# Kernel tuning notes

Measured on AMD Instinct MI355X. Metric: run time of the kernel, lower is better.

The kernel has to match this reference:

```python
import jax, jax.numpy as jnp
import numpy as np

N_MBED = 384
HEAD_SIZE = 64

def setup_inputs() -> dict:
    key = jax.random.key(0)
    kx, kq, kk, kv = jax.random.split(key, 4)
    B, T = 128, 256
    x = jax.random.normal(kx, (B, T, N_MBED), dtype=jnp.float32)
    # torch nn.Linear(n_mbed, head_size, bias=False): y = x @ W^T, W:[head_size, n_mbed].
    # We store the transposed weight [n_mbed, head_size] so y = x @ W.
    s = 1.0 / np.sqrt(N_MBED)
    Wq = jax.random.uniform(kq, (N_MBED, HEAD_SIZE), jnp.float32, -s, s)
    Wk = jax.random.uniform(kk, (N_MBED, HEAD_SIZE), jnp.float32, -s, s)
    Wv = jax.random.uniform(kv, (N_MBED, HEAD_SIZE), jnp.float32, -s, s)
    return {"x": x, "Wq": Wq, "Wk": Wk, "Wv": Wv}

def reference(x, Wq, Wk, Wv):
    B, T, C = x.shape  # C = n_mbed = 384
    q = x @ Wq  # [B,T,H]
    k = x @ Wk
    v = x @ Wv
    # Faithful to source: wei = k @ q^T, scaled by C**-0.5 (C = n_mbed, not head_size)
    wei = jnp.einsum('bth,bsh->bts', k, q) * (C ** -0.5)  # [B,T,T]
    mask = jnp.tril(jnp.ones((T, T), dtype=bool))
    wei = jnp.where(mask, wei, -jnp.inf)
    wei = jax.nn.softmax(wei, axis=-1)
    # dropout omitted (eval mode / identity)
    out = jnp.einsum('bts,bsh->bth', wei, v)  # [B,T,H]
    return out
```

## Files before the change

### kernel.cpp

```cpp
#include <hip/hip_runtime.h>
#include <hip/hip_bf16.h>
#include <math.h>

constexpr int kB = 128;
constexpr int kT = 256;
constexpr int kC = 384;
constexpr int kH = 64;

using bf16x8 = __attribute__((ext_vector_type(8))) short;
using f32x4  = __attribute__((ext_vector_type(4))) float;

union BF8 { bf16x8 v; __hip_bfloat162 h[4]; };
union BF4 { short4 s; __hip_bfloat162 h[2]; };

__device__ inline bf16x8 cvt8(float4 a, float4 b) {
    BF8 u;
    u.h[0] = __float22bfloat162_rn(float2{a.x, a.y});
    u.h[1] = __float22bfloat162_rn(float2{a.z, a.w});
    u.h[2] = __float22bfloat162_rn(float2{b.x, b.y});
    u.h[3] = __float22bfloat162_rn(float2{b.z, b.w});
    return u.v;
}
__device__ inline short4 cvt4(float4 a) {
    BF4 u;
    u.h[0] = __float22bfloat162_rn(float2{a.x, a.y});
    u.h[1] = __float22bfloat162_rn(float2{a.z, a.w});
    return u.s;
}
__device__ inline short bf1(float f) {
    __hip_bfloat16 h = __float2bfloat16(f);
    return *(short*)&h;
}

__global__ void prep_kernel(const float* __restrict__ Wq,
                            const float* __restrict__ Wk,
                            const float* __restrict__ Wv,
                            __hip_bfloat16* __restrict__ Wt) {
    int idx = blockIdx.x * 256 + threadIdx.x;
    int n = idx / kC, c = idx % kC;
    int w = n >> 6, h = n & 63;
    const float* W = (w == 0) ? Wq : (w == 1) ? Wk : Wv;
    float val = W[c * kH + h];
    if (w == 1) val *= 0.051031036307982884f;
    Wt[idx] = __float2bfloat16(val);
}

__global__ __launch_bounds__(512, 2) void fused_kernel(
    const float* __restrict__ x, const __hip_bfloat16* __restrict__ Wt,
    float* __restrict__ out)
{
    __shared__ short Qs[256 * 72];
    __shared__ short Ks[128 * 72];
    __shared__ short VTs[64 * 264];
    __shared__ short As[2][256 * 36];
    __shared__ short Bs[2][192 * 36];

    const int b    = blockIdx.y;
    const int half = (int)blockIdx.x ^ 1;
    const int t0   = half * 128;

    const int tid  = threadIdx.x;
    const int wave = tid >> 6, lane = tid & 63;
    const int m16  = lane & 15, quad = lane >> 4;
    const int wm = wave & 1, wn = wave >> 1;
    const short* wt = (const short*)Wt;
    const float* xb = x + (size_t)b * kT * kC;

    const bool mfmaAct = (half == 1) || (wm == 0);

    const int arow = tid >> 1, acol = (tid & 1) * 16;
    const bool aAct = (half == 1) || (arow < 128);

    float4 la[4]; bf16x8 lb0, lb1;
    auto glod = [&](int k0) {
        if (aAct) {
#pragma unroll
            for (int i = 0; i < 4; ++i)
                la[i] = *(const float4*)(xb + (size_t)arow * kC + k0 + acol + 4 * i);
        }
        {
            int n = tid >> 2, kk = (tid & 3) * 8;
            lb0 = *(const bf16x8*)(wt + (size_t)n * kC + k0 + kk);
        }
        if (tid < 256) {
            int c = tid + 512;
            int n = c >> 2, kk = (c & 3) * 8;
            lb1 = *(const bf16x8*)(wt + (size_t)n * kC + k0 + kk);
        }
    };
    auto swr = [&](int d) {
        if (aAct) {
#pragma unroll
            for (int i = 0; i < 4; ++i)
                *(short4*)&As[d][arow * 36 + acol + 4 * i] = cvt4(la[i]);
        }
        {
            int n = tid >> 2, kk = (tid & 3) * 8;
            *(bf16x8*)&Bs[d][n * 36 + kk] = lb0;
        }
        if (tid < 256) {
            int c = tid + 512;
            int n = c >> 2, kk = (c & 3) * 8;
            *(bf16x8*)&Bs[d][n * 36 + kk] = lb1;
        }
    };

    f32x4 acc[8][3];
#pragma unroll
    for (int mt = 0; mt < 8; ++mt)
#pragma unroll
        for (int j = 0; j < 3; ++j) acc[mt][j] = f32x4{0.f, 0.f, 0.f, 0.f};

    glod(0);
    swr(0);
    __syncthreads();

    for (int s = 0; s < 12; ++s) {
        const int d = s & 1;
        if (s < 11) glod((s + 1) * 32);

        if (mfmaAct) {
            bf16x8 af[8], bfr[3];
#pragma unroll
            for (int j = 0; j < 3; ++j)
                bfr[j] = *(const bf16x8*)&Bs[d][((wn * 3 + j) * 16 + m16) * 36 + quad * 8];
#pragma unroll
            for (int mt = 0; mt < 8; ++mt)
                af[mt] = *(const bf16x8*)&As[d][(wm * 128 + mt * 16 + m16) * 36 + quad * 8];
#pragma unroll
            for (int mt = 0; mt < 8; ++mt)
#pragma unroll
                for (int j = 0; j < 3; ++j)
                    acc[mt][j] = __builtin_amdgcn_mfma_f32_16x16x32_bf16(
                        af[mt], bfr[j], acc[mt][j], 0, 0, 0);
        }

        if (s < 11) swr(d ^ 1);
        __syncthreads();
    }

    if (mfmaAct) {
#pragma unroll
        for (int mt = 0; mt < 8; ++mt) {
            const int mbase = wm * 128 + mt * 16 + quad * 4;
#pragma unroll
            for (int j = 0; j < 3; ++j) {
                const int nt = wn * 3 + j;
                const int w  = nt >> 2;
                const int h  = (nt & 3) * 16 + m16;
                if (w == 2) {
                    float4 f = make_float4(acc[mt][j][0], acc[mt][j][1],
                                           acc[mt][j][2], acc[mt][j][3]);
                    *(short4*)&VTs[h * 264 + mbase] = cvt4(f);
                } else if (w == 1) {
                    if ((mbase >> 7) == half) {
#pragma unroll
                        for (int r = 0; r < 4; ++r)
                            Ks[(mbase + r - t0) * 72 + h] = bf1(acc[mt][j][r]);
                    }
                } else {
#pragma unroll
                    for (int r = 0; r < 4; ++r)
                        Qs[(mbase + r) * 72 + h] = bf1(acc[mt][j][r]);
                }
            }
        }
    }
    __syncthreads();

    const int wband = t0 + wave * 16;
    float* Pw = (float*)(&As[0][0]) + wave * 16 * 68;

    const bf16x8 ka0 = *(const bf16x8*)&Ks[(wave * 16 + m16) * 72 + quad * 8];
    const bf16x8 ka1 = *(const bf16x8*)&Ks[(wave * 16 + m16) * 72 + quad * 8 + 32];

    f32x4 O[4];
    float m_[4], l_[4];
#pragma unroll
    for (int i = 0; i < 4; ++i) {
        O[i] = f32x4{0.f, 0.f, 0.f, 0.f};
        m_[i] = -INFINITY; l_[i] = 0.f;
    }

    const int ilast = wband >> 6;
    for (int i = 0; i <= ilast; ++i) {
        const bool diag = (i == ilast);
        const int jmax = diag ? (wave & 3) : 3;

        f32x4 S[4];
        const f32x4 Z = f32x4{0.f, 0.f, 0.f, 0.f};
#pragma unroll
        for (int j = 0; j < 4; ++j) {
            if (j <= jmax) {
                bf16x8 qb0 = *(const bf16x8*)&Qs[(i * 64 + j * 16 + m16) * 72 + quad * 8];
                bf16x8 qb1 = *(const bf16x8*)&Qs[(i * 64 + j * 16 + m16) * 72 + quad * 8 + 32];
                S[j] = __builtin_amdgcn_mfma_f32_16x16x32_bf16(ka0, qb0, Z, 0, 0, 0);
                S[j] = __builtin_amdgcn_mfma_f32_16x16x32_bf16(ka1, qb1, S[j], 0, 0, 0);
            }
        }
        if (diag) {
#pragma unroll
            for (int r = 0; r < 4; ++r)
                if (m16 > quad * 4 + r) S[jmax][r] = -INFINITY;
        }

        float P[4][4];
#pragma unroll
        for (int j = 0; j < 4; ++j)
#pragma unroll
            for (int r = 0; r < 4; ++r) P[j][r] = 0.f;
#pragma unroll
        for (int r = 0; r < 4; ++r) {
            float rm = -INFINITY;
#pragma unroll
            for (int j = 0; j < 4; ++j)
                if (j <= jmax) rm = fmaxf(rm, S[j][r]);
            rm = fmaxf(rm, __shfl_xor(rm, 1, 64));
            rm = fmaxf(rm, __shfl_xor(rm, 2, 64));
            rm = fmaxf(rm, __shfl_xor(rm, 4, 64));
            rm = fmaxf(rm, __shfl_xor(rm, 8, 64));
            const float mn = fmaxf(m_[r], rm);
            const float al = __expf(m_[r] - mn);
            m_[r] = mn;
            float rs = 0.f;
#pragma unroll
            for (int j = 0; j < 4; ++j) {
                if (j <= jmax) { P[j][r] = __expf(S[j][r] - mn); rs += P[j][r]; }
            }
            rs += __shfl_xor(rs, 1, 64);
            rs += __shfl_xor(rs, 2, 64);
            rs += __shfl_xor(rs, 4, 64);
            rs += __shfl_xor(rs, 8, 64);
            l_[r] = l_[r] * al + rs;
            O[0][r] *= al; O[1][r] *= al; O[2][r] *= al; O[3][r] *= al;
        }

#pragma unroll
        for (int j = 0; j < 4; ++j)
#pragma unroll
            for (int r = 0; r < 4; ++r)
                Pw[(quad * 4 + r) * 68 + j * 16 + m16] = P[j][r];
        const float* pr = Pw + m16 * 68 + quad * 8;
        bf16x8 pf0 = cvt8(*(const float4*)pr,        *(const float4*)(pr + 4));
        bf16x8 pf1 = cvt8(*(const float4*)(pr + 32), *(const float4*)(pr + 36));

#pragma unroll
        for (int ht = 0; ht < 4; ++ht) {
            bf16x8 vb0 = *(const bf16x8*)&VTs[(ht * 16 + m16) * 264 + i * 64 + quad * 8];
            bf16x8 vb1 = *(const bf16x8*)&VTs[(ht * 16 + m16) * 264 + i * 64 + quad * 8 + 32];
            O[ht] = __builtin_amdgcn_mfma_f32_16x16x32_bf16(pf0, vb0, O[ht], 0, 0, 0);
            O[ht] = __builtin_amdgcn_mfma_f32_16x16x32_bf16(pf1, vb1, O[ht], 0, 0, 0);
        }
    }

#pragma unroll
    for (int r = 0; r < 4; ++r) {
        const float inv = 1.f / l_[r];
        const size_t row = (size_t)(b * kT + wband + quad * 4 + r);
#pragma unroll
        for (int ht = 0; ht < 4; ++ht)
            out[row * kH + ht * 16 + m16] = O[ht][r] * inv;
    }
}

extern "C" void kernel_launch(void* const* d_in, const int* in_sizes, int n_in,
                              void* d_out, int out_size, void* d_ws, size_t ws_size,
                              hipStream_t stream) {
    const float* x  = (const float*)d_in[0];
    const float* Wq = (const float*)d_in[1];
    const float* Wk = (const float*)d_in[2];
    const float* Wv = (const float*)d_in[3];
    float* out = (float*)d_out;

    __hip_bfloat16* Wt = (__hip_bfloat16*)d_ws;

    prep_kernel<<<(192 * kC) / 256, 256, 0, stream>>>(Wq, Wk, Wv, Wt);
    fused_kernel<<<dim3(2, kB), 512, 0, stream>>>(x, Wt, out);
}
```

Measured before the change: 117.0 us.

## Split fused projection+attention into separate projection and attention kernels via global bf16 QKV

Replaces the single fused kernel, where each block recomputed all 256 rows of Q/V projections for its half, with a projection kernel that computes Q, K and V^T per 64-row tile and writes them to global memory as bf16. A separate attention kernel then reads Q/K/V^T directly from global memory, handling 64 query rows per block with 256 threads. This removes the redundant projection work (each batch's Q and V were computed twice) and raises the block count and occupancy. It adds a global round trip for the intermediates, a second launch, and uncached global loads in the attention loop. P is now staged in shared memory as bf16 instead of fp32.

Result: slower. 122.1 us (+4.4%).

```diff
diff --git a/kernel.cpp b/kernel.cpp
--- a/kernel.cpp
+++ b/kernel.cpp
@@ -10,17 +10,8 @@
 using bf16x8 = __attribute__((ext_vector_type(8))) short;
 using f32x4  = __attribute__((ext_vector_type(4))) float;
 
-union BF8 { bf16x8 v; __hip_bfloat162 h[4]; };
 union BF4 { short4 s; __hip_bfloat162 h[2]; };
 
-__device__ inline bf16x8 cvt8(float4 a, float4 b) {
-    BF8 u;
-    u.h[0] = __float22bfloat162_rn(float2{a.x, a.y});
-    u.h[1] = __float22bfloat162_rn(float2{a.z, a.w});
-    u.h[2] = __float22bfloat162_rn(float2{b.x, b.y});
-    u.h[3] = __float22bfloat162_rn(float2{b.z, b.w});
-    return u.v;
-}
 __device__ inline short4 cvt4(float4 a) {
     BF4 u;
     u.h[0] = __float22bfloat162_rn(float2{a.x, a.y});
@@ -45,69 +36,49 @@
     Wt[idx] = __float2bfloat16(val);
 }
 
-__global__ __launch_bounds__(512, 2) void fused_kernel(
+__global__ __launch_bounds__(256, 4) void proj_kernel(
     const float* __restrict__ x, const __hip_bfloat16* __restrict__ Wt,
-    float* __restrict__ out)
+    short* __restrict__ Qg, short* __restrict__ Kg, short* __restrict__ VTg)
 {
-    __shared__ short Qs[256 * 72];
-    __shared__ short Ks[128 * 72];
-    __shared__ short VTs[64 * 264];
-    __shared__ short As[2][256 * 36];
+    __shared__ short As[2][64 * 36];
     __shared__ short Bs[2][192 * 36];
 
-    const int b    = blockIdx.y;
-    const int half = (int)blockIdx.x ^ 1;
-    const int t0   = half * 128;
+    const int bid = blockIdx.x;
+    const int b   = bid & 127;
+    const int q4  = bid >> 7;
+    const int row0 = b * kT + q4 * 64;
 
     const int tid  = threadIdx.x;
     const int wave = tid >> 6, lane = tid & 63;
     const int m16  = lane & 15, quad = lane >> 4;
-    const int wm = wave & 1, wn = wave >> 1;
     const short* wt = (const short*)Wt;
-    const float* xb = x + (size_t)b * kT * kC;
-
-    const bool mfmaAct = (half == 1) || (wm == 0);
-
-    const int arow = tid >> 1, acol = (tid & 1) * 16;
-    const bool aAct = (half == 1) || (arow < 128);
-
-    float4 la[4]; bf16x8 lb0, lb1;
+
+    const int arow = tid >> 2, acol = (tid & 3) * 8;
+    const float* xr = x + (size_t)(row0 + arow) * kC;
+
+    float4 la[2]; bf16x8 lb[3];
     auto glod = [&](int k0) {
-        if (aAct) {
-#pragma unroll
-            for (int i = 0; i < 4; ++i)
-                la[i] = *(const float4*)(xb + (size_t)arow * kC + k0 + acol + 4 * i);
-        }
-        {
-            int n = tid >> 2, kk = (tid & 3) * 8;
-            lb0 = *(const bf16x8*)(wt + (size_t)n * kC + k0 + kk);
-        }
-        if (tid < 256) {
-            int c = tid + 512;
-            int n = c >> 2, kk = (c & 3) * 8;
-            lb1 = *(const bf16x8*)(wt + (size_t)n * kC + k0 + kk);
+        la[0] = *(const float4*)(xr + k0 + acol);
+        la[1] = *(const float4*)(xr + k0 + acol + 4);
+#pragma unroll
+        for (int p = 0; p < 3; ++p) {
+            int c = tid + 256 * p, n = c >> 2, kk = (c & 3) * 8;
+            lb[p] = *(const bf16x8*)(wt + (size_t)n * kC + k0 + kk);
         }
     };
     auto swr = [&](int d) {
-        if (aAct) {
-#pragma unroll
-            for (int i = 0; i < 4; ++i)
-                *(short4*)&As[d][arow * 36 + acol + 4 * i] = cvt4(la[i]);
-        }
-        {
-            int n = tid >> 2, kk = (tid & 3) * 8;
-            *(bf16x8*)&Bs[d][n * 36 + kk] = lb0;
-        }
-        if (tid < 256) {
-            int c = tid + 512;
-            int n = c >> 2, kk = (c & 3) * 8;
-            *(bf16x8*)&Bs[d][n * 36 + kk] = lb1;
+        *(short4*)&As[d][arow * 36 + acol]     = cvt4(la[0]);
+        *(short4*)&As[d][arow * 36 + acol + 4] = cvt4(la[1]);
+#pragma unroll
+        for (int p = 0; p < 3; ++p) {
+            int c = tid + 256 * p, n = c >> 2, kk = (c & 3) * 8;
+            *(bf16x8*)&Bs[d][n * 36 + kk] = lb[p];
         }
     };
 
-    f32x4 acc[8][3];
-#pragma unroll
-    for (int mt = 0; mt < 8; ++mt)
+    f32x4 acc[4][3];
+#pragma unroll
+    for (int mt = 0; mt < 4; ++mt)
 #pragma unroll
         for (int j = 0; j < 3; ++j) acc[mt][j] = f32x4{0.f, 0.f, 0.f, 0.f};
 
@@ -119,60 +90,68 @@
         const int d = s & 1;
         if (s < 11) glod((s + 1) * 32);
 
-        if (mfmaAct) {
-            bf16x8 af[8], bfr[3];
-#pragma unroll
-            for (int j = 0; j < 3; ++j)
-                bfr[j] = *(const bf16x8*)&Bs[d][((wn * 3 + j) * 16 + m16) * 36 + quad * 8];
-#pragma unroll
-            for (int mt = 0; mt < 8; ++mt)
-                af[mt] = *(const bf16x8*)&As[d][(wm * 128 + mt * 16 + m16) * 36 + quad * 8];
-#pragma unroll
-            for (int mt = 0; mt < 8; ++mt)
-#pragma unroll
-                for (int j = 0; j < 3; ++j)
-                    acc[mt][j] = __builtin_amdgcn_mfma_f32_16x16x32_bf16(
-                        af[mt], bfr[j], acc[mt][j], 0, 0, 0);
+        bf16x8 af[4];
+#pragma unroll
+        for (int mt = 0; mt < 4; ++mt)
+            af[mt] = *(const bf16x8*)&As[d][(mt * 16 + m16) * 36 + quad * 8];
+#pragma unroll
+        for (int j = 0; j < 3; ++j) {
+            const bf16x8 bfr =
+                *(const bf16x8*)&Bs[d][((wave * 3 + j) * 16 + m16) * 36 + quad * 8];
+#pragma unroll
+            for (int mt = 0; mt < 4; ++mt)
+                acc[mt][j] = __builtin_amdgcn_mfma_f32_16x16x32_bf16(
+                    af[mt], bfr, acc[mt][j], 0, 0, 0);
         }
 
         if (s < 11) swr(d ^ 1);
         __syncthreads();
     }
 
-    if (mfmaAct) {
-#pragma unroll
-        for (int mt = 0; mt < 8; ++mt) {
-            const int mbase = wm * 128 + mt * 16 + quad * 4;
-#pragma unroll
-            for (int j = 0; j < 3; ++j) {
-                const int nt = wn * 3 + j;
-                const int w  = nt >> 2;
-                const int h  = (nt & 3) * 16 + m16;
-                if (w == 2) {
-                    float4 f = make_float4(acc[mt][j][0], acc[mt][j][1],
-                                           acc[mt][j][2], acc[mt][j][3]);
-                    *(short4*)&VTs[h * 264 + mbase] = cvt4(f);
-                } else if (w == 1) {
-                    if ((mbase >> 7) == half) {
-#pragma unroll
-                        for (int r = 0; r < 4; ++r)
-                            Ks[(mbase + r - t0) * 72 + h] = bf1(acc[mt][j][r]);
-                    }
-                } else {
-#pragma unroll
-                    for (int r = 0; r < 4; ++r)
-                        Qs[(mbase + r) * 72 + h] = bf1(acc[mt][j][r]);
-                }
+#pragma unroll
+    for (int mt = 0; mt < 4; ++mt) {
+        const int mrow = mt * 16 + quad * 4;
+#pragma unroll
+        for (int j = 0; j < 3; ++j) {
+            const int nt = wave * 3 + j;
+            const int w  = nt >> 2;
+            const int h  = (nt & 3) * 16 + m16;
+            if (w == 2) {
+                float4 f = make_float4(acc[mt][j][0], acc[mt][j][1],
+                                       acc[mt][j][2], acc[mt][j][3]);
+                *(short4*)&VTg[((size_t)b * kH + h) * kT + q4 * 64 + mrow] = cvt4(f);
+            } else {
+                short* G = (w == 1) ? Kg : Qg;
+#pragma unroll
+                for (int r = 0; r < 4; ++r)
+                    G[((size_t)b * kT + q4 * 64 + mrow + r) * kH + h] = bf1(acc[mt][j][r]);
             }
         }
     }
-    __syncthreads();
-
-    const int wband = t0 + wave * 16;
-    float* Pw = (float*)(&As[0][0]) + wave * 16 * 68;
-
-    const bf16x8 ka0 = *(const bf16x8*)&Ks[(wave * 16 + m16) * 72 + quad * 8];
-    const bf16x8 ka1 = *(const bf16x8*)&Ks[(wave * 16 + m16) * 72 + quad * 8 + 32];
+}
+
+__global__ __launch_bounds__(256, 4) void attn_kernel(
+    const short* __restrict__ Qg, const short* __restrict__ Kg,
+    const short* __restrict__ VTg, float* __restrict__ out)
+{
+    __shared__ short Pbuf[4][16 * 72];
+
+    const int bid = blockIdx.x;
+    const int b   = ((bid >> 5) << 3) | (bid & 7);
+    const int qi  = (bid >> 3) & 3;
+
+    const int tid  = threadIdx.x;
+    const int wave = tid >> 6, lane = tid & 63;
+    const int m16  = lane & 15, quad = lane >> 4;
+    const int trow0 = qi * 64 + wave * 16;
+
+    const short* Qb = Qg  + (size_t)b * kT * kH;
+    const short* Kb = Kg  + (size_t)b * kT * kH;
+    const short* Vb = VTg + (size_t)b * kH * kT;
+    short* Pb = Pbuf[wave];
+
+    const bf16x8 ka0 = *(const bf16x8*)&Kb[(trow0 + m16) * kH + quad * 8];
+    const bf16x8 ka1 = *(const bf16x8*)&Kb[(trow0 + m16) * kH + quad * 8 + 32];
 
     f32x4 O[4];
     float m_[4], l_[4];
@@ -182,18 +161,18 @@
         m_[i] = -INFINITY; l_[i] = 0.f;
     }
 
-    const int ilast = wband >> 6;
-    for (int i = 0; i <= ilast; ++i) {
-        const bool diag = (i == ilast);
-        const int jmax = diag ? (wave & 3) : 3;
+    for (int i = 0; i <= qi; ++i) {
+        const bool diag = (i == qi);
+        const int jmax = diag ? wave : 3;
 
         f32x4 S[4];
         const f32x4 Z = f32x4{0.f, 0.f, 0.f, 0.f};
 #pragma unroll
         for (int j = 0; j < 4; ++j) {
             if (j <= jmax) {
-                bf16x8 qb0 = *(const bf16x8*)&Qs[(i * 64 + j * 16 + m16) * 72 + quad * 8];
-                bf16x8 qb1 = *(const bf16x8*)&Qs[(i * 64 + j * 16 + m16) * 72 + quad * 8 + 32];
+                const int s = i * 64 + j * 16 + m16;
+                bf16x8 qb0 = *(const bf16x8*)&Qb[s * kH + quad * 8];
+                bf16x8 qb1 = *(const bf16x8*)&Qb[s * kH + quad * 8 + 32];
                 S[j] = __builtin_amdgcn_mfma_f32_16x16x32_bf16(ka0, qb0, Z, 0, 0, 0);
                 S[j] = __builtin_amdgcn_mfma_f32_16x16x32_bf16(ka1, qb1, S[j], 0, 0, 0);
             }
@@ -239,15 +218,14 @@
         for (int j = 0; j < 4; ++j)
 #pragma unroll
             for (int r = 0; r < 4; ++r)
-                Pw[(quad * 4 + r) * 68 + j * 16 + m16] = P[j][r];
-        const float* pr = Pw + m16 * 68 + quad * 8;
-        bf16x8 pf0 = cvt8(*(const float4*)pr,        *(const float4*)(pr + 4));
-        bf16x8 pf1 = cvt8(*(const float4*)(pr + 32), *(const float4*)(pr + 36));
+                Pb[(quad * 4 + r) * 72 + j * 16 + m16] = bf1(P[j][r]);
+        bf16x8 pf0 = *(const bf16x8*)&Pb[m16 * 72 + quad * 8];
+        bf16x8 pf1 = *(const bf16x8*)&Pb[m16 * 72 + quad * 8 + 32];
 
 #pragma unroll
         for (int ht = 0; ht < 4; ++ht) {
-            bf16x8 vb0 = *(const bf16x8*)&VTs[(ht * 16 + m16) * 264 + i * 64 + quad * 8];
-            bf16x8 vb1 = *(const bf16x8*)&VTs[(ht * 16 + m16) * 264 + i * 64 + quad * 8 + 32];
+            bf16x8 vb0 = *(const bf16x8*)&Vb[(ht * 16 + m16) * kT + i * 64 + quad * 8];
+            bf16x8 vb1 = *(const bf16x8*)&Vb[(ht * 16 + m16) * kT + i * 64 + quad * 8 + 32];
             O[ht] = __builtin_amdgcn_mfma_f32_16x16x32_bf16(pf0, vb0, O[ht], 0, 0, 0);
             O[ht] = __builtin_amdgcn_mfma_f32_16x16x32_bf16(pf1, vb1, O[ht], 0, 0, 0);
         }
@@ -256,7 +234,7 @@
 #pragma unroll
     for (int r = 0; r < 4; ++r) {
         const float inv = 1.f / l_[r];
-        const size_t row = (size_t)(b * kT + wband + quad * 4 + r);
+        const size_t row = (size_t)(b * kT + trow0 + quad * 4 + r);
 #pragma unroll
         for (int ht = 0; ht < 4; ++ht)
             out[row * kH + ht * 16 + m16] = O[ht][r] * inv;
@@ -272,8 +250,13 @@
     const float* Wv = (const float*)d_in[3];
     float* out = (float*)d_out;
 
-    __hip_bfloat16* Wt = (__hip_bfloat16*)d_ws;
+    short* base = (short*)d_ws;
+    __hip_bfloat16* Wt = (__hip_bfloat16*)base;
+    short* Qg  = base + 73728;
+    short* Kg  = Qg + (size_t)kB * kT * kH;
+    short* VTg = Kg + (size_t)kB * kT * kH;
 
     prep_kernel<<<(192 * kC) / 256, 256, 0, stream>>>(Wq, Wk, Wv, Wt);
-    fused_kernel<<<dim3(2, kB), 512, 0, stream>>>(x, Wt, out);
-}
+    proj_kernel<<<dim3(512), 256, 0, stream>>>(x, Wt, Qg, Kg, VTg);
+    attn_kernel<<<dim3(512), 256, 0, stream>>>(Qg, Kg, VTg, out);
+}
```
